# Performance work log

Measured on AMD Instinct MI355X. Metric: run time of the kernel, lower is better.

## Reference

```python
import jax, jax.numpy as jnp
import numpy as np

N, E, D, H, B = 50000, 100000, 768, 1, 16
NEG_SLOPE = 0.2  # DGL EdgeGATConv default negative_slope


def setup_inputs() -> dict:
    key = jax.random.key(0)
    ks = jax.random.split(key, 16)
    s = 1.0 / np.sqrt(D)  # CaseGNN.reset_parameters: uniform(-1/sqrt(h_dim), 1/sqrt(h_dim))
    u = lambda k, shp: jax.random.uniform(k, shp, jnp.float32, -s, s)
    node_feats = jax.random.normal(ks[0], (N, D), jnp.float32)
    edge_feats = jax.random.normal(ks[1], (E, D), jnp.float32)
    src = jax.random.randint(ks[2], (E,), 0, N)
    # guarantee every node has >=1 incoming edge (DGL disallows zero in-degree)
    dst = jnp.concatenate([jnp.arange(N), jax.random.randint(ks[3], (E - N,), 0, N)])
    graph_offsets = jnp.arange(B, dtype=jnp.int32) * (N // B)  # first node of each batched graph
    return dict(
        node_feats=node_feats, edge_feats=edge_feats, src=src, dst=dst,
        graph_offsets=graph_offsets,
        W1=u(ks[4], (D, H * D)), We1=u(ks[5], (D, H * D)),
        al1=u(ks[6], (H, D)), ar1=u(ks[7], (H, D)), ae1=u(ks[8], (H, D)),
        b1=u(ks[9], (H * D,)),
        W2=u(ks[10], (D, H * D)), We2=u(ks[11], (D, H * D)),
        al2=u(ks[12], (H, D)), ar2=u(ks[13], (H, D)), ae2=u(ks[14], (H, D)),
        b2=u(ks[15], (H * D,)),
    )


def _edge_gat(x, ef, src, dst, W, We, al, ar, ae, b):
    """DGL EdgeGATConv (num_heads=H, residual=Identity since in==H*out, bias=True)."""
    n = x.shape[0]
    fs = (x @ W).reshape(n, H, -1)               # [N,H,Do] projected node feats
    fe = (ef @ We).reshape(ef.shape[0], H, -1)   # [E,H,Do] projected edge feats
    el = jnp.sum(fs * al, axis=-1)               # [N,H]
    er = jnp.sum(fs * ar, axis=-1)               # [N,H]
    ee = jnp.sum(fe * ae, axis=-1)               # [E,H]
    e = jax.nn.leaky_relu(el[src] + er[dst] + ee, NEG_SLOPE)  # [E,H]
    # edge_softmax over incoming edges of each dst node (numerically stable)
    emax = jax.ops.segment_max(e, dst, num_segments=n)
    emax = jnp.where(jnp.isfinite(emax), emax, 0.0)
    w = jnp.exp(e - emax[dst])
    wsum = jax.ops.segment_sum(w, dst, num_segments=n)[dst]
    a = w / jnp.where(wsum > 0, wsum, 1.0)       # [E,H]
    m = (fs[src] + fe) * a[..., None]            # [E,H,Do] messages
    rst = jax.ops.segment_sum(m, dst, num_segments=n)  # [N,H,Do]
    rst = rst + x.reshape(n, H, -1)              # identity residual
    rst = rst + b.reshape(1, H, -1)
    return rst.reshape(n, -1)                    # th.squeeze (H=1)


def reference(node_feats, edge_feats, src, dst, graph_offsets,
              W1, We1, al1, ar1, ae1, b1, W2, We2, al2, ar2, ae2, b2):
    h = _edge_gat(node_feats, edge_feats, src, dst, W1, We1, al1, ar1, ae1, b1)
    h = jax.nn.relu(h)  # dropouts are identity at eval
    h = _edge_gat(h, edge_feats, src, dst, W2, We2, al2, ar2, ae2, b2)
    return h[graph_offsets]  # first-node embedding of each graph, [B, D]
```

## Files before the change

kernel.cpp:

```cpp
#include <hip/hip_runtime.h>

#define D 768
#define CAP 64
#define MD1 16
#define MAXROWS 1040
#define VROWS 64
#define QCAP 64
#define NI 24
#define IC 32
#define NEG 0.2f

__device__ __forceinline__ float wave_reduce(float v) {
    #pragma unroll
    for (int o = 32; o > 0; o >>= 1) v += __shfl_down(v, o, 64);
    return v;
}

__global__ __launch_bounds__(256) void k1_zero_proj(
        const float* W1, const float* We1, const float* W2, const float* We2,
        const float* al1, const float* ar1, const float* ae1,
        const float* al2, const float* ar2, const float* ae2,
        int* zspan, int nzero, float* v) {
    if (blockIdx.x == 0)
        for (int i = threadIdx.x; i < nzero; i += 256) zspan[i] = 0;
    int task = blockIdx.x * 4 + (threadIdx.x >> 6);
    int lane = threadIdx.x & 63;
    if (task >= 4 * D) return;
    int g = task / D, i = task % D;
    const float* W; const float* p1; const float* p2 = nullptr; int o1 = 0, o2 = 0;
    switch (g) {
        case 0: W = W1;  p1 = al1; p2 = ar1; o1 = 0;     o2 = D;     break;
        case 1: W = We1; p1 = ae1;           o1 = 2 * D;             break;
        case 2: W = W2;  p1 = al2; p2 = ar2; o1 = 3 * D; o2 = 4 * D; break;
        default:W = We2; p1 = ae2;           o1 = 5 * D;             break;
    }
    float s1 = 0.f, s2 = 0.f;
    for (int j = lane; j < D; j += 64) {
        float w = W[(long)i * D + j];
        s1 += w * p1[j];
        if (p2) s2 += w * p2[j];
    }
    #pragma unroll
    for (int o = 32; o > 0; o >>= 1) { s1 += __shfl_down(s1, o, 64); s2 += __shfl_down(s2, o, 64); }
    if (lane == 0) { v[o1 + i] = s1; if (p2) v[o2 + i] = s2; }
}

__global__ __launch_bounds__(256) void k2_build(
        const int* __restrict__ dst, const int* __restrict__ goff,
        int E, int B, int* l2e, int* cnt) {
    __shared__ int tg[32];
    if ((int)threadIdx.x < B) tg[threadIdx.x] = goff[threadIdx.x];
    __syncthreads();
    for (int e = blockIdx.x * 256 + threadIdx.x; e < E; e += gridDim.x * 256) {
        int d = dst[e];
        for (int b = 0; b < B; ++b) {
            if (d == tg[b]) {
                int pos = atomicAdd(&cnt[b], 1);
                if (pos < CAP) l2e[b * CAP + pos] = e;
            }
        }
    }
}

__global__ __launch_bounds__(256) void k3_match(
        const float* __restrict__ x, const float* __restrict__ ef,
        const int* __restrict__ src, const int* __restrict__ dst,
        const int* __restrict__ goff, const int* __restrict__ l2e,
        const int* __restrict__ cnt, const float* __restrict__ b1,
        const float* __restrict__ v, int E, int B, int nslot,
        int* mcnt, int* medge, int* msrc, float* melog, float* erj, float* h) {
    __shared__ int tnode[MAXROWS], tslot[MAXROWS];
    __shared__ int tn, qn;
    __shared__ int qe[QCAP], qs[QCAP], qsl[QCAP], qp[QCAP];
    int tid = threadIdx.x;
    if (tid == 0) { tn = 0; qn = 0; }
    __syncthreads();
    for (int s = tid; s < nslot; s += 256) {
        int node = -1; bool valid = false;
        if (s < B) { node = goff[s]; valid = true; }
        else { int rb = (s - B) >> 6, i = (s - B) & 63;
               int cb = cnt[rb]; if (cb > CAP) cb = CAP;
               if (i < cb) { node = src[l2e[rb * CAP + i]]; valid = true; } }
        if (valid) { int p = atomicAdd(&tn, 1); tnode[p] = node; tslot[p] = s; }
    }
    __syncthreads();
    int M = tn;
    const float* val1 = v;
    const float* var1 = v + D;
    const float* vae1 = v + 2 * D;
    {
        int wv = tid >> 6, lane = tid & 63;
        int s = blockIdx.x * 4 + wv;
        if (s < nslot) {
            int j = -1; bool valid = false;
            if (s < B) { j = goff[s]; valid = true; }
            else { int rb = (s - B) >> 6, i = (s - B) & 63;
                   int cb = cnt[rb]; if (cb > CAP) cb = CAP;
                   if (i < cb) { j = src[l2e[rb * CAP + i]]; valid = true; } }
            if (valid) {
                float acc = 0.f;
                for (int c = lane; c < D; c += 64) acc += x[(long)j * D + c] * var1[c];
                acc = wave_reduce(acc);
                if (lane == 0) erj[s] = acc;
                for (int c = lane; c < D; c += 64)
                    h[(long)s * D + c] = x[(long)j * D + c] + b1[c];
            }
        }
    }
    for (int e = blockIdx.x * 256 + tid; e < E; e += gridDim.x * 256) {
        int d = dst[e];
        for (int c = 0; c < M; ++c) {
            if (tnode[c] == d) {
                int sl = tslot[c];
                int p = atomicAdd(&mcnt[sl], 1);
                if (p < MD1) {
                    int sr = src[e];
                    medge[sl * MD1 + p] = e;
                    msrc[sl * MD1 + p] = sr;
                    int qq = atomicAdd(&qn, 1);
                    if (qq < QCAP) { qe[qq] = e; qs[qq] = sr; qsl[qq] = sl; qp[qq] = p; }
                    else {
                        float acc = 0.f;
                        for (int cc = 0; cc < D; ++cc)
                            acc += x[(long)sr * D + cc] * val1[cc] + ef[(long)e * D + cc] * vae1[cc];
                        melog[sl * MD1 + p] = acc;
                    }
                }
            }
        }
    }
    __syncthreads();
    int nq = qn; if (nq > QCAP) nq = QCAP;
    int wv = tid >> 6, lane = tid & 63;
    for (int m = wv; m < nq; m += 4) {
        int e = qe[m], sr = qs[m];
        float acc = 0.f;
        for (int c = lane; c < D; c += 64)
            acc += x[(long)sr * D + c] * val1[c] + ef[(long)e * D + c] * vae1[c];
        acc = wave_reduce(acc);
        if (lane == 0) melog[qsl[m] * MD1 + qp[m]] = acc;
    }
}

__global__ __launch_bounds__(256) void k4_gemm1(
        const float* __restrict__ W1, const float* __restrict__ We1,
        const float* __restrict__ x, const float* __restrict__ ef,
        const int* __restrict__ cnt, const int* __restrict__ mcnt,
        const int* __restrict__ medge, const int* __restrict__ msrc,
        const float* __restrict__ melog, const float* __restrict__ erj,
        float* h, int B, int nslot) {
    __shared__ int vl[VROWS];
    __shared__ int vn_sh, snm[VROWS];
    __shared__ float smatt[VROWS][MD1];
    __shared__ int ssrc[VROWS][MD1], sedge[VROWS][MD1];
    __shared__ float scs[4][IC], ecs[4][IC];
    int tid = threadIdx.x;
    int q = blockIdx.x % 3, iy = blockIdx.x / 3;
    int col = q * 256 + tid, i0 = iy * IC;
    float w[IC], we[IC];
    #pragma unroll
    for (int k = 0; k < IC; ++k) {
        w[k]  = W1[(long)(i0 + k) * D + col];
        we[k] = We1[(long)(i0 + k) * D + col];
    }
    if (tid < 64) {
        int base = 0;
        for (int s0 = 0; s0 < nslot; s0 += 64) {
            int s = s0 + tid;
            bool valid = false;
            if (s < B) valid = true;
            else if (s < nslot) {
                int rb = (s - B) >> 6, i = (s - B) & 63;
                int cb = cnt[rb]; if (cb > CAP) cb = CAP;
                valid = i < cb;
            }
            unsigned long long mb = __ballot(valid);
            if (valid) {
                int ci = base + __popcll(mb & ((1ULL << tid) - 1));
                if (ci < VROWS) vl[ci] = s;
            }
            base += __popcll(mb);
        }
        if (tid == 0) vn_sh = base < VROWS ? base : VROWS;
    }
    __syncthreads();
    int vn = vn_sh;
    if (tid < vn) {
        int s = vl[tid];
        int nm = mcnt[s]; if (nm > MD1) nm = MD1;
        snm[tid] = nm;
        for (int k = 0; k < nm; ++k) {
            sedge[tid][k] = medge[s * MD1 + k];
            ssrc[tid][k]  = msrc[s * MD1 + k];
            smatt[tid][k] = melog[s * MD1 + k];
        }
        for (int a_ = 1; a_ < nm; ++a_) {
            int ke = sedge[tid][a_], ks = ssrc[tid][a_]; float kl = smatt[tid][a_];
            int b = a_ - 1;
            while (b >= 0 && sedge[tid][b] > ke) {
                sedge[tid][b+1] = sedge[tid][b]; ssrc[tid][b+1] = ssrc[tid][b];
                smatt[tid][b+1] = smatt[tid][b]; --b;
            }
            sedge[tid][b+1] = ke; ssrc[tid][b+1] = ks; smatt[tid][b+1] = kl;
        }
        float er = erj[s], mx = -1e30f;
        for (int k = 0; k < nm; ++k) {
            float l = smatt[tid][k] + er;
            l = l >= 0.f ? l : NEG * l;
            smatt[tid][k] = l; mx = fmaxf(mx, l);
        }
        float sum = 0.f;
        for (int k = 0; k < nm; ++k) { float p = expf(smatt[tid][k] - mx); smatt[tid][k] = p; sum += p; }
        float inv = 1.f / sum;
        for (int k = 0; k < nm; ++k) smatt[tid][k] *= inv;
    }
    __syncthreads();
    int wv = tid >> 6, lane = tid & 63;
    for (int g = 0; g < vn; g += 4) {
        int r = g + wv;
        if (r < vn) {
            int nm = snm[r];
            if (lane < IC) {
                float a = 0.f;
                for (int k = 0; k < nm; ++k)
                    a += smatt[r][k] * x[(long)ssrc[r][k] * D + i0 + lane];
                scs[wv][lane] = a;
            } else {
                float a = 0.f;
                for (int k = 0; k < nm; ++k)
                    a += smatt[r][k] * ef[(long)sedge[r][k] * D + i0 + lane - IC];
                ecs[wv][lane - IC] = a;
            }
        }
        __syncthreads();
        int gmax = vn - g; if (gmax > 4) gmax = 4;
        for (int rr = 0; rr < gmax; ++rr) {
            float acc = 0.f;
            #pragma unroll
            for (int k = 0; k < IC; ++k) acc += scs[rr][k] * w[k] + ecs[rr][k] * we[k];
            atomicAdd(&h[(long)vl[g + rr] * D + col], acc);
        }
        __syncthreads();
    }
}

__global__ __launch_bounds__(256) void k5_l2prep(
        const float* __restrict__ ef, const int* __restrict__ l2e,
        const int* __restrict__ cnt, const float* __restrict__ b2,
        const float* __restrict__ v, const float* __restrict__ h,
        float* elog2, float* er2, float* out, int B, int nslot) {
    int wv = threadIdx.x >> 6, lane = threadIdx.x & 63;
    int t = blockIdx.x * 4 + wv;
    const float* val2 = v + 3 * D;
    const float* var2 = v + 4 * D;
    const float* vae2 = v + 5 * D;
    if (t < B) {
        float acc = 0.f;
        for (int c = lane; c < D; c += 64) acc += fmaxf(h[(long)t * D + c], 0.f) * var2[c];
        acc = wave_reduce(acc);
        if (lane == 0) er2[t] = acc;
        for (int c = lane; c < D; c += 64)
            out[(long)t * D + c] = fmaxf(h[(long)t * D + c], 0.f) + b2[c];
    } else if (t < nslot) {
        int rb = (t - B) >> 6, i = (t - B) & 63;
        int cb = cnt[rb]; if (cb > CAP) cb = CAP;
        if (i < cb) {
            int e = l2e[rb * CAP + i];
            const float* hs = h + (long)t * D;
            float acc = 0.f;
            for (int c = lane; c < D; c += 64)
                acc += fmaxf(hs[c], 0.f) * val2[c] + ef[(long)e * D + c] * vae2[c];
            acc = wave_reduce(acc);
            if (lane == 0) elog2[rb * CAP + i] = acc;
        }
    }
}

__global__ __launch_bounds__(256) void k6_gemm2(
        const float* __restrict__ W2, const float* __restrict__ We2,
        const float* __restrict__ ef, const int* __restrict__ l2e,
        const int* __restrict__ cnt, const float* __restrict__ elog2,
        const float* __restrict__ er2, const float* __restrict__ h,
        float* out, int B) {
    __shared__ float smatt[16][CAP];
    __shared__ int sedge[16][CAP], spos[16][CAP], sdeg[16];
    __shared__ float scs[4][IC], ecs[4][IC];
    int tid = threadIdx.x;
    int q = blockIdx.x % 3, iy = blockIdx.x / 3;
    int col = q * 256 + tid, i0 = iy * IC;
    float w[IC], we[IC];
    #pragma unroll
    for (int k = 0; k < IC; ++k) {
        w[k]  = W2[(long)(i0 + k) * D + col];
        we[k] = We2[(long)(i0 + k) * D + col];
    }
    if (tid < B) {
        int b = tid;
        int deg = cnt[b]; if (deg > CAP) deg = CAP;
        sdeg[b] = deg;
        for (int k = 0; k < deg; ++k) { sedge[b][k] = l2e[b * CAP + k]; spos[b][k] = k; }
        for (int a_ = 1; a_ < deg; ++a_) {
            int ke = sedge[b][a_], kp = spos[b][a_]; int c = a_ - 1;
            while (c >= 0 && sedge[b][c] > ke) {
                sedge[b][c+1] = sedge[b][c]; spos[b][c+1] = spos[b][c]; --c;
            }
            sedge[b][c+1] = ke; spos[b][c+1] = kp;
        }
        float er = er2[b], mx = -1e30f;
        for (int k = 0; k < deg; ++k) {
            float l = elog2[b * CAP + spos[b][k]] + er;
            l = l >= 0.f ? l : NEG * l;
            smatt[b][k] = l; mx = fmaxf(mx, l);
        }
        float sum = 0.f;
        for (int k = 0; k < deg; ++k) { float p = expf(smatt[b][k] - mx); smatt[b][k] = p; sum += p; }
        float inv = 1.f / sum;
        for (int k = 0; k < deg; ++k) smatt[b][k] *= inv;
    }
    __syncthreads();
    int wv = tid >> 6, lane = tid & 63;
    for (int g = 0; g < B; g += 4) {
        int b = g + wv;
        int deg = sdeg[b];
        if (lane < IC) {
            float a = 0.f;
            for (int k = 0; k < deg; ++k)
                a += smatt[b][k] * fmaxf(h[(long)(B + b * CAP + spos[b][k]) * D + i0 + lane], 0.f);
            scs[wv][lane] = a;
        } else {
            float a = 0.f;
            for (int k = 0; k < deg; ++k)
                a += smatt[b][k] * ef[(long)sedge[b][k] * D + i0 + lane - IC];
            ecs[wv][lane - IC] = a;
        }
        __syncthreads();
        for (int rr = 0; rr < 4; ++rr) {
            float acc = 0.f;
            #pragma unroll
            for (int k = 0; k < IC; ++k) acc += scs[rr][k] * w[k] + ecs[rr][k] * we[k];
            atomicAdd(&out[(long)(g + rr) * D + col], acc);
        }
        __syncthreads();
    }
}

extern "C" void kernel_launch(void* const* d_in, const int* in_sizes, int n_in,
                              void* d_out, int out_size, void* d_ws, size_t ws_size,
                              hipStream_t stream) {
    const float* x    = (const float*)d_in[0];
    const float* ef   = (const float*)d_in[1];
    const int*   src  = (const int*)d_in[2];
    const int*   dst  = (const int*)d_in[3];
    const int*   goff = (const int*)d_in[4];
    const float* W1   = (const float*)d_in[5];
    const float* We1  = (const float*)d_in[6];
    const float* al1  = (const float*)d_in[7];
    const float* ar1  = (const float*)d_in[8];
    const float* ae1  = (const float*)d_in[9];
    const float* b1   = (const float*)d_in[10];
    const float* W2   = (const float*)d_in[11];
    const float* We2  = (const float*)d_in[12];
    const float* al2  = (const float*)d_in[13];
    const float* ar2  = (const float*)d_in[14];
    const float* ae2  = (const float*)d_in[15];
    const float* b2   = (const float*)d_in[16];
    float* out = (float*)d_out;

    int E = in_sizes[2];
    int B = in_sizes[4];
    int nslot = B + B * CAP;

    float* ws    = (float*)d_ws;
    float* v     = ws;
    int*   l2e   = (int*)(v + 6 * D);
    int*   cnt   = l2e + B * CAP;
    int*   mcnt  = cnt + B;
    int*   medge = mcnt + nslot;
    int*   msrc  = medge + nslot * MD1;
    float* melog = (float*)(msrc + nslot * MD1);
    float* erj   = melog + nslot * MD1;
    float* elog2 = erj + nslot;
    float* er2   = elog2 + B * CAP;
    float* h     = er2 + B;

    int nzero = B + nslot;
    int egrid = (E + 255) / 256;

    hipLaunchKernelGGL(k1_zero_proj, dim3(4 * D / 4), dim3(256), 0, stream,
                       W1, We1, W2, We2, al1, ar1, ae1, al2, ar2, ae2, cnt, nzero, v);
    hipLaunchKernelGGL(k2_build, dim3(egrid), dim3(256), 0, stream,
                       dst, goff, E, B, l2e, cnt);
    hipLaunchKernelGGL(k3_match, dim3(egrid), dim3(256), 0, stream,
                       x, ef, src, dst, goff, l2e, cnt, b1, v, E, B, nslot,
                       mcnt, medge, msrc, melog, erj, h);
    hipLaunchKernelGGL(k4_gemm1, dim3(3 * NI), dim3(256), 0, stream,
                       W1, We1, x, ef, cnt, mcnt, medge, msrc, melog, erj, h, B, nslot);
    hipLaunchKernelGGL(k5_l2prep, dim3((nslot + 3) / 4), dim3(256), 0, stream,
                       ef, l2e, cnt, b2, v, h, elog2, er2, out, B, nslot);
    hipLaunchKernelGGL(k6_gemm2, dim3(3 * NI), dim3(256), 0, stream,
                       W2, We2, ef, l2e, cnt, elog2, er2, h, out, B);
}
```

Measured before the change: 88.76 us.

## Fuse layer-2 logit prep into gemm2 and move valid-row compaction into match kernel

Merges the separate layer-2 prep kernel into the second GEMM kernel. Every GEMM block now recomputes the per-edge attention logits and the destination term with wave reductions, and the output zeroing moves into the first kernel. The valid-row list compaction moves from every gemm1 block into block 0 of the match kernel and is passed through global memory. Both GEMMs now gather all rows into shared memory once, with a thread per row/matrix over 32 columns, then accumulate, instead of syncing per group of 4 rows. This removes one launch and many barriers, but each of the 72 gemm2 blocks repeats the logit reductions, and the per-thread strided 32-float loads are uncoalesced.

```diff
diff --git a/kernel.cpp b/kernel.cpp
--- a/kernel.cpp
+++ b/kernel.cpp
@@ -20,9 +20,11 @@
         const float* W1, const float* We1, const float* W2, const float* We2,
         const float* al1, const float* ar1, const float* ae1,
         const float* al2, const float* ar2, const float* ae2,
-        int* zspan, int nzero, float* v) {
+        int* zspan, int nzero, float* outz, int nout, float* v) {
     if (blockIdx.x == 0)
         for (int i = threadIdx.x; i < nzero; i += 256) zspan[i] = 0;
+    if (blockIdx.x == 1)
+        for (int i = threadIdx.x; i < nout; i += 256) outz[i] = 0.f;
     int task = blockIdx.x * 4 + (threadIdx.x >> 6);
     int lane = threadIdx.x & 63;
     if (task >= 4 * D) return;
@@ -68,7 +70,8 @@
         const int* __restrict__ goff, const int* __restrict__ l2e,
         const int* __restrict__ cnt, const float* __restrict__ b1,
         const float* __restrict__ v, int E, int B, int nslot,
-        int* mcnt, int* medge, int* msrc, float* melog, float* erj, float* h) {
+        int* mcnt, int* medge, int* msrc, float* melog, float* erj, float* h,
+        int* vlg, int* vnp) {
     __shared__ int tnode[MAXROWS], tslot[MAXROWS];
     __shared__ int tn, qn;
     __shared__ int qe[QCAP], qs[QCAP], qsl[QCAP], qp[QCAP];
@@ -140,30 +143,7 @@
         acc = wave_reduce(acc);
         if (lane == 0) melog[qsl[m] * MD1 + qp[m]] = acc;
     }
-}
-
-__global__ __launch_bounds__(256) void k4_gemm1(
-        const float* __restrict__ W1, const float* __restrict__ We1,
-        const float* __restrict__ x, const float* __restrict__ ef,
-        const int* __restrict__ cnt, const int* __restrict__ mcnt,
-        const int* __restrict__ medge, const int* __restrict__ msrc,
-        const float* __restrict__ melog, const float* __restrict__ erj,
-        float* h, int B, int nslot) {
-    __shared__ int vl[VROWS];
-    __shared__ int vn_sh, snm[VROWS];
-    __shared__ float smatt[VROWS][MD1];
-    __shared__ int ssrc[VROWS][MD1], sedge[VROWS][MD1];
-    __shared__ float scs[4][IC], ecs[4][IC];
-    int tid = threadIdx.x;
-    int q = blockIdx.x % 3, iy = blockIdx.x / 3;
-    int col = q * 256 + tid, i0 = iy * IC;
-    float w[IC], we[IC];
-    #pragma unroll
-    for (int k = 0; k < IC; ++k) {
-        w[k]  = W1[(long)(i0 + k) * D + col];
-        we[k] = We1[(long)(i0 + k) * D + col];
-    }
-    if (tid < 64) {
+    if (blockIdx.x == 0 && tid < 64) {
         int base = 0;
         for (int s0 = 0; s0 < nslot; s0 += 64) {
             int s = s0 + tid;
@@ -177,16 +157,41 @@
             unsigned long long mb = __ballot(valid);
             if (valid) {
                 int ci = base + __popcll(mb & ((1ULL << tid) - 1));
-                if (ci < VROWS) vl[ci] = s;
+                if (ci < VROWS) vlg[ci] = s;
             }
             base += __popcll(mb);
         }
-        if (tid == 0) vn_sh = base < VROWS ? base : VROWS;
-    }
-    __syncthreads();
-    int vn = vn_sh;
+        if (tid == 0) *vnp = base < VROWS ? base : VROWS;
+    }
+}
+
+__global__ __launch_bounds__(256) void k4_gemm1(
+        const float* __restrict__ W1, const float* __restrict__ We1,
+        const float* __restrict__ x, const float* __restrict__ ef,
+        const int* __restrict__ mcnt, const int* __restrict__ medge,
+        const int* __restrict__ msrc, const float* __restrict__ melog,
+        const float* __restrict__ erj, const int* __restrict__ vlg,
+        const int* __restrict__ vnp, float* h) {
+    int tid = threadIdx.x;
+    int q = blockIdx.x % 3, iy = blockIdx.x / 3;
+    int col = q * 256 + tid, i0 = iy * IC;
+    float w[IC], we[IC];
+    #pragma unroll
+    for (int k = 0; k < IC; ++k) {
+        w[k]  = W1[(long)(i0 + k) * D + col];
+        we[k] = We1[(long)(i0 + k) * D + col];
+    }
+    __shared__ int vl_s[VROWS];
+    __shared__ int vn_s, snm[VROWS];
+    __shared__ float smatt[VROWS][MD1];
+    __shared__ int ssrc[VROWS][MD1], sedge[VROWS][MD1];
+    __shared__ float sgS[VROWS][IC], sgE[VROWS][IC];
+    if (tid == 0) vn_s = *vnp;
+    if (tid < VROWS) vl_s[tid] = vlg[tid];
+    __syncthreads();
+    int vn = vn_s;
     if (tid < vn) {
-        int s = vl[tid];
+        int s = vl_s[tid];
         int nm = mcnt[s]; if (nm > MD1) nm = MD1;
         snm[tid] = nm;
         for (int k = 0; k < nm; ++k) {
@@ -215,76 +220,47 @@
         for (int k = 0; k < nm; ++k) smatt[tid][k] *= inv;
     }
     __syncthreads();
-    int wv = tid >> 6, lane = tid & 63;
-    for (int g = 0; g < vn; g += 4) {
-        int r = g + wv;
-        if (r < vn) {
-            int nm = snm[r];
-            if (lane < IC) {
-                float a = 0.f;
-                for (int k = 0; k < nm; ++k)
-                    a += smatt[r][k] * x[(long)ssrc[r][k] * D + i0 + lane];
-                scs[wv][lane] = a;
-            } else {
-                float a = 0.f;
-                for (int k = 0; k < nm; ++k)
-                    a += smatt[r][k] * ef[(long)sedge[r][k] * D + i0 + lane - IC];
-                ecs[wv][lane - IC] = a;
-            }
-        }
-        __syncthreads();
-        int gmax = vn - g; if (gmax > 4) gmax = 4;
-        for (int rr = 0; rr < gmax; ++rr) {
-            float acc = 0.f;
+    for (int t = tid; t < 2 * vn; t += 256) {
+        int r = t >> 1, mat = t & 1;
+        int nm = snm[r];
+        float acc[IC];
+        #pragma unroll
+        for (int i = 0; i < IC; ++i) acc[i] = 0.f;
+        if (mat == 0) {
+            for (int k = 0; k < nm; ++k) {
+                const float* p = x + (long)ssrc[r][k] * D + i0;
+                float a_ = smatt[r][k];
+                #pragma unroll
+                for (int i = 0; i < IC; ++i) acc[i] += a_ * p[i];
+            }
             #pragma unroll
-            for (int k = 0; k < IC; ++k) acc += scs[rr][k] * w[k] + ecs[rr][k] * we[k];
-            atomicAdd(&h[(long)vl[g + rr] * D + col], acc);
-        }
-        __syncthreads();
-    }
-}
-
-__global__ __launch_bounds__(256) void k5_l2prep(
+            for (int i = 0; i < IC; ++i) sgS[r][i] = acc[i];
+        } else {
+            for (int k = 0; k < nm; ++k) {
+                const float* p = ef + (long)sedge[r][k] * D + i0;
+                float a_ = smatt[r][k];
+                #pragma unroll
+                for (int i = 0; i < IC; ++i) acc[i] += a_ * p[i];
+            }
+            #pragma unroll
+            for (int i = 0; i < IC; ++i) sgE[r][i] = acc[i];
+        }
+    }
+    __syncthreads();
+    for (int r = 0; r < vn; ++r) {
+        float acc = 0.f;
+        #pragma unroll
+        for (int k = 0; k < IC; ++k) acc += sgS[r][k] * w[k] + sgE[r][k] * we[k];
+        atomicAdd(&h[(long)vl_s[r] * D + col], acc);
+    }
+}
+
+__global__ __launch_bounds__(256) void k5_gemm2(
+        const float* __restrict__ W2, const float* __restrict__ We2,
         const float* __restrict__ ef, const int* __restrict__ l2e,
         const int* __restrict__ cnt, const float* __restrict__ b2,
         const float* __restrict__ v, const float* __restrict__ h,
-        float* elog2, float* er2, float* out, int B, int nslot) {
-    int wv = threadIdx.x >> 6, lane = threadIdx.x & 63;
-    int t = blockIdx.x * 4 + wv;
-    const float* val2 = v + 3 * D;
-    const float* var2 = v + 4 * D;
-    const float* vae2 = v + 5 * D;
-    if (t < B) {
-        float acc = 0.f;
-        for (int c = lane; c < D; c += 64) acc += fmaxf(h[(long)t * D + c], 0.f) * var2[c];
-        acc = wave_reduce(acc);
-        if (lane == 0) er2[t] = acc;
-        for (int c = lane; c < D; c += 64)
-            out[(long)t * D + c] = fmaxf(h[(long)t * D + c], 0.f) + b2[c];
-    } else if (t < nslot) {
-        int rb = (t - B) >> 6, i = (t - B) & 63;
-        int cb = cnt[rb]; if (cb > CAP) cb = CAP;
-        if (i < cb) {
-            int e = l2e[rb * CAP + i];
-            const float* hs = h + (long)t * D;
-            float acc = 0.f;
-            for (int c = lane; c < D; c += 64)
-                acc += fmaxf(hs[c], 0.f) * val2[c] + ef[(long)e * D + c] * vae2[c];
-            acc = wave_reduce(acc);
-            if (lane == 0) elog2[rb * CAP + i] = acc;
-        }
-    }
-}
-
-__global__ __launch_bounds__(256) void k6_gemm2(
-        const float* __restrict__ W2, const float* __restrict__ We2,
-        const float* __restrict__ ef, const int* __restrict__ l2e,
-        const int* __restrict__ cnt, const float* __restrict__ elog2,
-        const float* __restrict__ er2, const float* __restrict__ h,
         float* out, int B) {
-    __shared__ float smatt[16][CAP];
-    __shared__ int sedge[16][CAP], spos[16][CAP], sdeg[16];
-    __shared__ float scs[4][IC], ecs[4][IC];
     int tid = threadIdx.x;
     int q = blockIdx.x % 3, iy = blockIdx.x / 3;
     int col = q * 256 + tid, i0 = iy * IC;
@@ -294,6 +270,13 @@
         w[k]  = W2[(long)(i0 + k) * D + col];
         we[k] = We2[(long)(i0 + k) * D + col];
     }
+    __shared__ int sedge[16][CAP], spos[16][CAP], sdeg[16];
+    __shared__ float slog[16][CAP], ser[16];
+    __shared__ int pref[17];
+    __shared__ float sgS[16][IC], sgE[16][IC];
+    const float* val2 = v + 3 * D;
+    const float* var2 = v + 4 * D;
+    const float* vae2 = v + 5 * D;
     if (tid < B) {
         int b = tid;
         int deg = cnt[b]; if (deg > CAP) deg = CAP;
@@ -306,41 +289,83 @@
             }
             sedge[b][c+1] = ke; spos[b][c+1] = kp;
         }
-        float er = er2[b], mx = -1e30f;
+    }
+    __syncthreads();
+    if (tid == 0) {
+        pref[0] = 0;
+        for (int b = 0; b < B; ++b) pref[b + 1] = pref[b] + sdeg[b];
+    }
+    __syncthreads();
+    int ntask = B + pref[B];
+    int wv = tid >> 6, lane = tid & 63;
+    for (int t = wv; t < ntask; t += 4) {
+        if (t < B) {
+            const float* hb = h + (long)t * D;
+            float acc = 0.f;
+            for (int c = lane; c < D; c += 64) acc += fmaxf(hb[c], 0.f) * var2[c];
+            acc = wave_reduce(acc);
+            if (lane == 0) ser[t] = acc;
+        } else {
+            int et = t - B;
+            int b = 0;
+            while (pref[b + 1] <= et) ++b;
+            int k = et - pref[b];
+            int e = sedge[b][k];
+            const float* hs = h + (long)(B + b * CAP + spos[b][k]) * D;
+            float acc = 0.f;
+            for (int c = lane; c < D; c += 64)
+                acc += fmaxf(hs[c], 0.f) * val2[c] + ef[(long)e * D + c] * vae2[c];
+            acc = wave_reduce(acc);
+            if (lane == 0) slog[b][k] = acc;
+        }
+    }
+    __syncthreads();
+    if (tid < B) {
+        int b = tid, deg = sdeg[b];
+        float er = ser[b], mx = -1e30f;
         for (int k = 0; k < deg; ++k) {
-            float l = elog2[b * CAP + spos[b][k]] + er;
+            float l = slog[b][k] + er;
             l = l >= 0.f ? l : NEG * l;
-            smatt[b][k] = l; mx = fmaxf(mx, l);
+            slog[b][k] = l; mx = fmaxf(mx, l);
         }
         float sum = 0.f;
-        for (int k = 0; k < deg; ++k) { float p = expf(smatt[b][k] - mx); smatt[b][k] = p; sum += p; }
-        float inv = 1.f / sum;
-        for (int k = 0; k < deg; ++k) smatt[b][k] *= inv;
-    }
-    __syncthreads();
-    int wv = tid >> 6, lane = tid & 63;
-    for (int g = 0; g < B; g += 4) {
-        int b = g + wv;
-        int deg = sdeg[b];
-        if (lane < IC) {
-            float a = 0.f;
-            for (int k = 0; k < deg; ++k)
-                a += smatt[b][k] * fmaxf(h[(long)(B + b * CAP + spos[b][k]) * D + i0 + lane], 0.f);
-            scs[wv][lane] = a;
+        for (int k = 0; k < deg; ++k) { float p = expf(slog[b][k] - mx); slog[b][k] = p; sum += p; }
+        float inv = sum > 0.f ? 1.f / sum : 0.f;
+        for (int k = 0; k < deg; ++k) slog[b][k] *= inv;
+    }
+    __syncthreads();
+    for (int t = tid; t < 2 * B; t += 256) {
+        int r = t >> 1, mat = t & 1;
+        int deg = sdeg[r];
+        float acc[IC];
+        #pragma unroll
+        for (int i = 0; i < IC; ++i) acc[i] = 0.f;
+        if (mat == 0) {
+            for (int k = 0; k < deg; ++k) {
+                const float* hs = h + (long)(B + r * CAP + spos[r][k]) * D + i0;
+                float a_ = slog[r][k];
+                #pragma unroll
+                for (int i = 0; i < IC; ++i) acc[i] += a_ * fmaxf(hs[i], 0.f);
+            }
+            #pragma unroll
+            for (int i = 0; i < IC; ++i) sgS[r][i] = acc[i];
         } else {
-            float a = 0.f;
-            for (int k = 0; k < deg; ++k)
-                a += smatt[b][k] * ef[(long)sedge[b][k] * D + i0 + lane - IC];
-            ecs[wv][lane - IC] = a;
-        }
-        __syncthreads();
-        for (int rr = 0; rr < 4; ++rr) {
-            float acc = 0.f;
+            for (int k = 0; k < deg; ++k) {
+                const float* p = ef + (long)sedge[r][k] * D + i0;
+                float a_ = slog[r][k];
+                #pragma unroll
+                for (int i = 0; i < IC; ++i) acc[i] += a_ * p[i];
+            }
             #pragma unroll
-            for (int k = 0; k < IC; ++k) acc += scs[rr][k] * w[k] + ecs[rr][k] * we[k];
-            atomicAdd(&out[(long)(g + rr) * D + col], acc);
-        }
-        __syncthreads();
+            for (int i = 0; i < IC; ++i) sgE[r][i] = acc[i];
+        }
+    }
+    __syncthreads();
+    for (int r = 0; r < B; ++r) {
+        float acc = (iy == 0) ? fmaxf(h[(long)r * D + col], 0.f) + b2[col] : 0.f;
+        #pragma unroll
+        for (int k = 0; k < IC; ++k) acc += sgS[r][k] * w[k] + sgE[r][k] * we[k];
+        atomicAdd(&out[(long)r * D + col], acc);
     }
 }
 
@@ -379,24 +404,23 @@
     int*   msrc  = medge + nslot * MD1;
     float* melog = (float*)(msrc + nslot * MD1);
     float* erj   = melog + nslot * MD1;
-    float* elog2 = erj + nslot;
-    float* er2   = elog2 + B * CAP;
-    float* h     = er2 + B;
+    int*   vlg   = (int*)(erj + nslot);
+    int*   vnp   = vlg + VROWS;
+    float* h     = (float*)(vnp + 1);
 
     int nzero = B + nslot;
     int egrid = (E + 255) / 256;
 
     hipLaunchKernelGGL(k1_zero_proj, dim3(4 * D / 4), dim3(256), 0, stream,
-                       W1, We1, W2, We2, al1, ar1, ae1, al2, ar2, ae2, cnt, nzero, v);
+                       W1, We1, W2, We2, al1, ar1, ae1, al2, ar2, ae2,
+                       cnt, nzero, out, B * D, v);
     hipLaunchKernelGGL(k2_build, dim3(egrid), dim3(256), 0, stream,
                        dst, goff, E, B, l2e, cnt);
     hipLaunchKernelGGL(k3_match, dim3(egrid), dim3(256), 0, stream,
                        x, ef, src, dst, goff, l2e, cnt, b1, v, E, B, nslot,
-                       mcnt, medge, msrc, melog, erj, h);
+                       mcnt, medge, msrc, melog, erj, h, vlg, vnp);
     hipLaunchKernelGGL(k4_gemm1, dim3(3 * NI), dim3(256), 0, stream,
-                       W1, We1, x, ef, cnt, mcnt, medge, msrc, melog, erj, h, B, nslot);
-    hipLaunchKernelGGL(k5_l2prep, dim3((nslot + 3) / 4), dim3(256), 0, stream,
-                       ef, l2e, cnt, b2, v, h, elog2, er2, out, B, nslot);
-    hipLaunchKernelGGL(k6_gemm2, dim3(3 * NI), dim3(256), 0, stream,
-                       W2, We2, ef, l2e, cnt, elog2, er2, h, out, B);
-}
+                       W1, We1, x, ef, mcnt, medge, msrc, melog, erj, vlg, vnp, h);
+    hipLaunchKernelGGL(k5_gemm2, dim3(3 * NI), dim3(256), 0, stream,
+                       W2, We2, ef, l2e, cnt, b2, v, h, out, B);
+}
```

Measured after the change: 110.1 us. +24.1%, slower.
